# Optimization experiments

Hardware: AMD Instinct MI355X
Metric: run time of the kernel (lower is better)

Reference implementation:

```python
import jax, jax.numpy as jnp
import numpy as np

N, E, T = 50000, 200000, 100000
D, H, C = 512, 512, 7
BN_EPS = 1e-5


def _bn(h, g, b):
    # BatchNorm1d with batch statistics (training-mode stats, biased var as torch)
    m = jnp.mean(h, axis=0)
    v = jnp.var(h, axis=0)
    return (h - m) * jax.lax.rsqrt(v + BN_EPS) * g + b


def _forward(x, graph, edge_index, train_edge_id,
             W_sub, bn1_g, bn1_b, fcx_W, fcx_b, eps1,
             g_W1, g_b1, g_W2, g_b2, gbn_g, gbn_b,
             lin1_W, lin1_b, lin2_W, lin2_b, fc2_W, fc2_b):
    src, dst = edge_index[0], edge_index[1]
    n = x.shape[0]

    # SubgraphGNNKernel approximation: one GINConv (eps=0), mlp_layers=1 linear
    # (bias=False per bias=False), residual add (res=True)
    agg_s = graph + jax.ops.segment_sum(graph[src], dst, num_segments=n)
    sub_x = agg_s @ W_sub + graph  # [N, D]
    sub_x = jax.nn.relu(_bn(sub_x, bn1_g, bn1_b))  # dropout: eval no-op

    # fc_x
    h = x @ fcx_W + fcx_b  # [N, D]

    # GINConv: mlp((1+eps)*h + sum_{j->i} h_j)
    agg = (1.0 + eps1) * h + jax.ops.segment_sum(h[src], dst, num_segments=n)
    h = jax.nn.relu(agg @ g_W1 + g_b1)
    h = jax.nn.relu(h @ g_W2 + g_b2)
    h = _bn(h, gbn_g, gbn_b)  # [N, H]

    # lin1 -> relu -> (dropout eval no-op) -> lin2, add subgraph branch
    h = jax.nn.relu(h @ lin1_W + lin1_b)
    h = h @ lin2_W + lin2_b
    h = h + sub_x  # [N, H]

    # link prediction: gather endpoints of training edges, elementwise mul
    nid = edge_index[:, train_edge_id]  # [2, T]
    pair = h[nid[0]] * h[nid[1]]  # [T, H]
    return pair @ fc2_W + fc2_b  # [T, C]


def setup_inputs() -> dict:
    key = jax.random.key(0)
    ks = jax.random.split(key, 20)
    w = lambda k, shape: (jax.random.normal(k, shape, jnp.float32)
                          * (1.0 / np.sqrt(shape[0])))
    return {
        "x": jax.random.normal(ks[0], (N, D), jnp.float32),
        "graph": jax.random.normal(ks[1], (N, D), jnp.float32),
        "edge_index": jax.random.randint(ks[2], (2, E), 0, N),
        "train_edge_id": jax.random.randint(ks[3], (T,), 0, E),
        "W_sub": w(ks[4], (D, D)),
        "bn1_g": jnp.ones((D,), jnp.float32),
        "bn1_b": jnp.zeros((D,), jnp.float32),
        "fcx_W": w(ks[5], (D, D)),
        "fcx_b": jnp.zeros((D,), jnp.float32),
        "eps1": jnp.zeros((), jnp.float32),
        "g_W1": w(ks[6], (D, H)),
        "g_b1": jnp.zeros((H,), jnp.float32),
        "g_W2": w(ks[7], (H, H)),
        "g_b2": jnp.zeros((H,), jnp.float32),
        "gbn_g": jnp.ones((H,), jnp.float32),
        "gbn_b": jnp.zeros((H,), jnp.float32),
        "lin1_W": w(ks[8], (H, H)),
        "lin1_b": jnp.zeros((H,), jnp.float32),
        "lin2_W": w(ks[9], (H, H)),
        "lin2_b": jnp.zeros((H,), jnp.float32),
        "fc2_W": w(ks[10], (H, C)),
        "fc2_b": jnp.zeros((C,), jnp.float32),
    }


def reference(x, graph, edge_index, train_edge_id,
              W_sub, bn1_g, bn1_b, fcx_W, fcx_b, eps1,
              g_W1, g_b1, g_W2, g_b2, gbn_g, gbn_b,
              lin1_W, lin1_b, lin2_W, lin2_b, fc2_W, fc2_b):
    return _forward(x, graph, edge_index, train_edge_id,
                    W_sub, bn1_g, bn1_b, fcx_W, fcx_b, eps1,
                    g_W1, g_b1, g_W2, g_b2, gbn_g, gbn_b,
                    lin1_W, lin1_b, lin2_W, lin2_b, fc2_W, fc2_b)
```

## Files before the change

kernel.cpp:

```cpp
#include <hip/hip_runtime.h>

#define N_NODES 50000
#define N_EDGES 200000
#define N_TRAIN 100000
#define DIM     512
#define NCLS    7
#define NSB     ((N_NODES + 255) / 256)

typedef unsigned short ushort;
typedef _Float16 f16x8 __attribute__((ext_vector_type(8)));
typedef float    f32x4 __attribute__((ext_vector_type(4)));

__device__ __forceinline__ ushort f2h(float f) {
    _Float16 h = (_Float16)f;
    union { _Float16 h; ushort u; } v; v.h = h; return v.u;
}
__device__ __forceinline__ float h2f(ushort u) {
    union { ushort u; _Float16 h; } v; v.u = u; return (float)v.h;
}

__device__ __forceinline__ void gload_lds16(const void* g, void* l) {
    __builtin_amdgcn_global_load_lds((const __attribute__((address_space(1))) unsigned int*)g,
                                     (__attribute__((address_space(3))) unsigned int*)l,
                                     16, 0, 0);
}

#define VMWAIT(N) asm volatile("s_waitcnt vmcnt(" #N ")" ::: "memory")
#define LGKM0()   asm volatile("s_waitcnt lgkmcnt(0)" ::: "memory")
#define BAR() do { asm volatile("" ::: "memory"); __builtin_amdgcn_s_barrier(); \
                   asm volatile("" ::: "memory"); } while (0)


__global__ void zero_kernel(float* p, int n) {
    int i = blockIdx.x * blockDim.x + threadIdx.x;
    if (i < n) p[i] = 0.0f;
}


__global__ void hist_kernel(const int* __restrict__ ei, int* __restrict__ cnt) {
    int e = blockIdx.x * blockDim.x + threadIdx.x;
    if (e < N_EDGES) atomicAdd(&cnt[ei[N_EDGES + e]], 1);
}

__global__ __launch_bounds__(256) void scan1_kernel(const int* __restrict__ cnt,
                                                    int* __restrict__ off,
                                                    int* __restrict__ bsum) {
    __shared__ int s[256];
    int t = threadIdx.x, b = blockIdx.x;
    int i = b * 256 + t;
    s[t] = (i < N_NODES) ? cnt[i] : 0;
    __syncthreads();
    for (int d = 1; d < 256; d <<= 1) {
        int add = (t >= d) ? s[t - d] : 0;
        __syncthreads();
        s[t] += add;
        __syncthreads();
    }
    if (i < N_NODES) off[i + 1] = s[t];
    if (t == 255) bsum[b] = s[255];
}

__global__ __launch_bounds__(256) void scan2_kernel(int* bsum) {
    __shared__ int s[256];
    int t = threadIdx.x;
    s[t] = (t < NSB) ? bsum[t] : 0;
    __syncthreads();
    for (int d = 1; d < 256; d <<= 1) {
        int add = (t >= d) ? s[t - d] : 0;
        __syncthreads();
        s[t] += add;
        __syncthreads();
    }
    if (t < NSB) bsum[t] = s[t];
}

__global__ __launch_bounds__(256) void scan3_kernel(int* off, const int* __restrict__ bsum) {
    int t = threadIdx.x, b = blockIdx.x;
    int i = b * 256 + t;
    if (i == 0) off[0] = 0;
    if (i < N_NODES) off[i + 1] += (b > 0 ? bsum[b - 1] : 0);
}

__global__ void fillprep_kernel(const int* __restrict__ off, int* __restrict__ wcur) {
    int i = blockIdx.x * blockDim.x + threadIdx.x;
    if (i < N_NODES) wcur[i] = off[i];
}

__global__ void fill_kernel(const int* __restrict__ ei, int* __restrict__ wcur,
                            int* __restrict__ srclist) {
    int e = blockIdx.x * blockDim.x + threadIdx.x;
    if (e < N_EDGES) {
        int d = ei[N_EDGES + e];
        int pos = atomicAdd(&wcur[d], 1);
        srclist[pos] = ei[e];
    }
}


__global__ __launch_bounds__(128) void gather_h_kernel(const float* __restrict__ feat,
                                                       const float* __restrict__ base,
                                                       const float* eps_or_null,
                                                       const int* __restrict__ off,
                                                       const int* __restrict__ srclist,
                                                       ushort* __restrict__ oh) {
    int n = blockIdx.x;
    int t = threadIdx.x;
    float s = 1.0f;
    if (eps_or_null) s = 1.0f + *eps_or_null;
    int e0 = off[n], e1 = off[n + 1];
    float4 acc = ((const float4*)(base + (size_t)n * DIM))[t];
    acc.x *= s; acc.y *= s; acc.z *= s; acc.w *= s;
    for (int e = e0; e < e1; ++e) {
        int srcn = srclist[e];
        float4 v = ((const float4*)(feat + (size_t)srcn * DIM))[t];
        acc.x += v.x; acc.y += v.y; acc.z += v.z; acc.w += v.w;
    }
    size_t o = (size_t)n * DIM + t * 4;
    ushort4 r;
    r.x = f2h(acc.x); r.y = f2h(acc.y); r.z = f2h(acc.z); r.w = f2h(acc.w);
    *(ushort4*)(oh + o) = r;
}


__global__ __launch_bounds__(128) void gather_h16_kernel(const ushort* __restrict__ feat,
                                                         const ushort* __restrict__ base,
                                                         const float* eps_or_null,
                                                         const int* __restrict__ off,
                                                         const int* __restrict__ srclist,
                                                         ushort* __restrict__ oh) {
    int n = blockIdx.x;
    int t = threadIdx.x;
    float s = 1.0f;
    if (eps_or_null) s = 1.0f + *eps_or_null;
    int e0 = off[n], e1 = off[n + 1];
    ushort4 b4 = ((const ushort4*)(base + (size_t)n * DIM))[t];
    float4 acc;
    acc.x = h2f(b4.x) * s; acc.y = h2f(b4.y) * s;
    acc.z = h2f(b4.z) * s; acc.w = h2f(b4.w) * s;
    for (int e = e0; e < e1; ++e) {
        int srcn = srclist[e];
        ushort4 v = ((const ushort4*)(feat + (size_t)srcn * DIM))[t];
        acc.x += h2f(v.x); acc.y += h2f(v.y); acc.z += h2f(v.z); acc.w += h2f(v.w);
    }
    size_t o = (size_t)n * DIM + t * 4;
    ushort4 r;
    r.x = f2h(acc.x); r.y = f2h(acc.y); r.z = f2h(acc.z); r.w = f2h(acc.w);
    *(ushort4*)(oh + o) = r;
}

__global__ void convert_h_kernel(const float* __restrict__ X,
                                 ushort* __restrict__ oh, size_t n4) {
    size_t i = (size_t)blockIdx.x * blockDim.x + threadIdx.x;
    size_t stride = (size_t)gridDim.x * blockDim.x;
    const float4* X4 = (const float4*)X;
    for (; i < n4; i += stride) {
        float4 v = X4[i];
        ushort4 r;
        r.x = f2h(v.x); r.y = f2h(v.y); r.z = f2h(v.z); r.w = f2h(v.w);
        *(ushort4*)(oh + i * 4) = r;
    }
}

__global__ void wconvert6_kernel(const float* __restrict__ W0, const float* __restrict__ W1,
                                 const float* __restrict__ W2, const float* __restrict__ W3,
                                 const float* __restrict__ W4, const float* __restrict__ W5,
                                 ushort* __restrict__ wt) {
    int p = blockIdx.y;
    const float* W = (p == 0) ? W0 : (p == 1) ? W1 : (p == 2) ? W2
                   : (p == 3) ? W3 : (p == 4) ? W4 : W5;
    ushort* Th = wt + (size_t)p * 262144;
    int idx = blockIdx.x * 256 + threadIdx.x;
    int n = idx >> 9, k = idx & 511;
    Th[idx] = f2h(W[k * DIM + n]);
}

__global__ void wfold_kernel(const float* __restrict__ W1, const float* __restrict__ st2,
                             ushort* __restrict__ lw1s) {
    int idx = blockIdx.x * 256 + threadIdx.x;
    int n = idx >> 9, k = idx & 511;
    lw1s[idx] = f2h(W1[k * DIM + n] * st2[1024 + k]);
}

__global__ void bfold_kernel(const float* __restrict__ W1, const float* __restrict__ b1,
                             const float* __restrict__ st2, float* __restrict__ b1f) {
    int c = threadIdx.x;
    float s = 0.f;
#pragma unroll 8
    for (int k = 0; k < DIM; k++) s += st2[1536 + k] * W1[k * DIM + c];
    b1f[c] = b1[c] + s;
}


__global__ __launch_bounds__(512, 6) void gemm_f16_kernel(
    const ushort* __restrict__ Ahp0, const ushort* __restrict__ Wf0,
    const float* __restrict__ bias0, const float* __restrict__ amf0,
    const ushort* __restrict__ amh0, const float* __restrict__ bnst0,
    float* __restrict__ Cf0, ushort* __restrict__ Oh0, float* __restrict__ stats0,
    int relu0, int mode0,
    const ushort* __restrict__ Ahp1, const ushort* __restrict__ Wf1,
    const float* __restrict__ bias1, const float* __restrict__ amf1,
    const ushort* __restrict__ amh1, const float* __restrict__ bnst1,
    float* __restrict__ Cf1, ushort* __restrict__ Oh1, float* __restrict__ stats1,
    int relu1, int mode1,
    int M)
{
    __shared__ __align__(16) char smem[3 * 16384];

    const ushort* Ahp; const ushort* Wf; const float* bias; const float* addmat_f;
    const ushort* addmat_h; const float* bnst; float* Cf; ushort* Oh; float* stats;
    int relu, mode;
    if (blockIdx.y == 0) {
        Ahp = Ahp0; Wf = Wf0; bias = bias0; addmat_f = amf0; addmat_h = amh0;
        bnst = bnst0; Cf = Cf0; Oh = Oh0; stats = stats0; relu = relu0; mode = mode0;
    } else {
        Ahp = Ahp1; Wf = Wf1; bias = bias1; addmat_f = amf1; addmat_h = amh1;
        bnst = bnst1; Cf = Cf1; Oh = Oh1; stats = stats1; relu = relu1; mode = mode1;
    }

    int tid = threadIdx.x;
    int w = tid >> 6;
    int l = tid & 63;
    int wm = w >> 2;
    int wn = w & 3;

    int nwg = gridDim.x;
    int q = nwg >> 3, r = nwg & 7;
    int xcd = blockIdx.x & 7, idx = blockIdx.x >> 3;
    int wgid = (xcd < r ? xcd * (q + 1) : r * (q + 1) + (xcd - r) * q) + idx;
    int bm = (wgid >> 2) * 128;
    int bn = (wgid & 3) * 128;

    f32x4 acc[4][2];
#pragma unroll
    for (int i = 0; i < 4; i++)
#pragma unroll
        for (int j = 0; j < 2; j++) acc[i][j] = (f32x4){0.f, 0.f, 0.f, 0.f};

    int ro = l & 15;
    int co = l >> 4;

    size_t soff[2]; int lofs[2];
#pragma unroll
    for (int t2 = 0; t2 < 2; t2++) {
        int c = 2 * w + t2;
        int row0, base_; bool cl;
        if (c < 8) { row0 = c * 16;       base_ = bm; cl = true;  lofs[t2] = c * 1024; }
        else       { row0 = (c - 8) * 16; base_ = bn; cl = false; lofs[t2] = 8192 + (c - 8) * 1024; }
        int lrit = row0 + (l >> 2);
        int rr = base_ + lrit;
        if (cl) rr = min(rr, M - 1);
        int kc = (l & 3) ^ ((lrit >> 1) & 3);
        soff[t2] = (size_t)rr * DIM + kc * 8;
    }
    const ushort* sp0 = (2 * w < 8) ? Ahp : Wf;
    const ushort* sp1 = (2 * w + 1 < 8) ? Ahp : Wf;

    int aoff[4], woff[2];
#pragma unroll
    for (int i = 0; i < 4; i++) {
        int arow = wm * 64 + i * 16 + ro;
        aoff[i] = arow * 64 + ((co ^ ((arow >> 1) & 3)) << 4);
    }
#pragma unroll
    for (int j = 0; j < 2; j++) {
        int wrow = wn * 32 + j * 16 + ro;
        woff[j] = 8192 + wrow * 64 + ((co ^ ((wrow >> 1) & 3)) << 4);
    }

#define STAGE(BB, K0) do {                                                        \
    char* sb_ = smem + (BB) * 16384;                                              \
    gload_lds16(sp0 + soff[0] + (K0), sb_ + lofs[0]);                             \
    gload_lds16(sp1 + soff[1] + (K0), sb_ + lofs[1]);                             \
} while (0)

#define COMPUTE(BB) do {                                                          \
    const char* bb_ = (const char*)smem + (BB) * 16384;                           \
    f16x8 fa[4], fw2[2];                                                          \
    _Pragma("unroll")                                                             \
    for (int i = 0; i < 4; i++) fa[i] = *(const f16x8*)(bb_ + aoff[i]);           \
    _Pragma("unroll")                                                             \
    for (int j = 0; j < 2; j++) fw2[j] = *(const f16x8*)(bb_ + woff[j]);          \
    __builtin_amdgcn_s_setprio(1);                                                \
    _Pragma("unroll")                                                             \
    for (int i = 0; i < 4; i++)                                                   \
        _Pragma("unroll")                                                         \
        for (int j = 0; j < 2; j++)                                               \
            acc[i][j] = __builtin_amdgcn_mfma_f32_16x16x32_f16(fa[i], fw2[j], acc[i][j], 0, 0, 0); \
    __builtin_amdgcn_s_setprio(0);                                                \
} while (0)

    STAGE(0, 0);
    STAGE(1, 32);
    STAGE(2, 64);

    int bufi = 0;
    for (int ks = 0; ks < 16; ks++) {
        if (ks < 14)      { VMWAIT(4); }
        else if (ks == 14){ VMWAIT(2); }
        else              { VMWAIT(0); }
        BAR();
        COMPUTE(bufi);
        LGKM0();
        BAR();
        if (ks <= 12) STAGE(bufi, (ks + 3) * 32);
        bufi = (bufi == 2) ? 0 : bufi + 1;
    }

#undef STAGE
#undef COMPUTE

    int colbase = bn + wn * 32 + ro;
    int rowbase = bm + wm * 64 + co * 4;
    float sacc[2] = {0.f, 0.f};
    float qacc[2] = {0.f, 0.f};
#pragma unroll
    for (int j = 0; j < 2; j++) {
        int col = colbase + j * 16;
        float bi = bias ? bias[col] : 0.f;
        float sc = 0.f, sh = 0.f;
        if (bnst) { sc = bnst[1024 + col]; sh = bnst[1536 + col]; }
#pragma unroll
        for (int i = 0; i < 4; i++) {
#pragma unroll
            for (int rg = 0; rg < 4; rg++) {
                int row = rowbase + i * 16 + rg;
                if (row < M) {
                    float v = acc[i][j][rg] + bi;
                    if (addmat_f || addmat_h) {
                        float am = addmat_f ? addmat_f[(size_t)row * DIM + col]
                                            : h2f(addmat_h[(size_t)row * DIM + col]);
                        if (bnst) am = fmaxf(am * sc + sh, 0.f);
                        v += am;
                    }
                    if (relu) v = fmaxf(v, 0.f);
                    if (mode == 0) Cf[(size_t)row * DIM + col] = v;
                    else           Oh[(size_t)row * DIM + col] = f2h(v);
                    if (stats) { sacc[j] += v; qacc[j] += v * v; }
                }
            }
        }
    }
    if (stats) {
#pragma unroll
        for (int j = 0; j < 2; j++) {
            float ss = sacc[j], qq = qacc[j];
            ss += __shfl_xor(ss, 16); qq += __shfl_xor(qq, 16);
            ss += __shfl_xor(ss, 32); qq += __shfl_xor(qq, 32);
            if (co == 0) {
                int col = colbase + j * 16;
                atomicAdd(&stats[col], ss);
                atomicAdd(&stats[DIM + col], qq);
            }
        }
    }
}


__global__ void bn_finalize_kernel(float* st, const float* __restrict__ g,
                                   const float* __restrict__ b, int M) {
    int c = threadIdx.x;
    float mean = st[c] / (float)M;
    float var = st[DIM + c] / (float)M - mean * mean;
    float sc = g[c] * rsqrtf(var + 1e-5f);
    st[1024 + c] = sc;
    st[1536 + c] = b[c] - mean * sc;
}


__global__ __launch_bounds__(256) void pair_kernel(const ushort* __restrict__ H,
                                                   const int* __restrict__ ei,
                                                   const int* __restrict__ teid,
                                                   const float* __restrict__ W,
                                                   const float* __restrict__ bias,
                                                   float* __restrict__ out) {
    int lane = threadIdx.x & 63;
    int wid = blockIdx.x * 4 + (threadIdx.x >> 6);
    int nw = gridDim.x * 4;
    int d0 = lane * 8;

    float wreg[8][NCLS];
#pragma unroll
    for (int qd = 0; qd < 8; qd++)
#pragma unroll
        for (int c = 0; c < NCLS; c++)
            wreg[qd][c] = W[(d0 + qd) * NCLS + c];
    float bi[NCLS];
#pragma unroll
    for (int c = 0; c < NCLS; c++) bi[c] = bias[c];

    for (int t = wid; t < N_TRAIN; t += nw) {
        int id = teid[t];
        int n0 = ei[id];
        int n1 = ei[N_EDGES + id];
        f16x8 av = *(const f16x8*)(H + (size_t)n0 * DIM + d0);
        f16x8 bv = *(const f16x8*)(H + (size_t)n1 * DIM + d0);
        float acc[NCLS];
#pragma unroll
        for (int c = 0; c < NCLS; c++) acc[c] = 0.f;
#pragma unroll
        for (int qd = 0; qd < 8; qd++) {
            float p = (float)av[qd] * (float)bv[qd];
#pragma unroll
            for (int c = 0; c < NCLS; c++) acc[c] += p * wreg[qd][c];
        }
#pragma unroll
        for (int off = 32; off; off >>= 1)
#pragma unroll
            for (int c = 0; c < NCLS; c++) acc[c] += __shfl_down(acc[c], off);
        if (lane == 0) {
#pragma unroll
            for (int c = 0; c < NCLS; c++) out[(size_t)t * NCLS + c] = acc[c] + bi[c];
        }
    }
}


extern "C" void kernel_launch(void* const* d_in, const int* in_sizes, int n_in,
                              void* d_out, int out_size, void* d_ws, size_t ws_size,
                              hipStream_t stream) {
    const float* x      = (const float*)d_in[0];
    const float* graph  = (const float*)d_in[1];
    const int*   ei     = (const int*)d_in[2];
    const int*   teid   = (const int*)d_in[3];
    const float* W_sub  = (const float*)d_in[4];
    const float* bn1_g  = (const float*)d_in[5];
    const float* bn1_b  = (const float*)d_in[6];
    const float* fcx_W  = (const float*)d_in[7];
    const float* fcx_b  = (const float*)d_in[8];
    const float* eps1   = (const float*)d_in[9];
    const float* g_W1   = (const float*)d_in[10];
    const float* g_b1   = (const float*)d_in[11];
    const float* g_W2   = (const float*)d_in[12];
    const float* g_b2   = (const float*)d_in[13];
    const float* gbn_g  = (const float*)d_in[14];
    const float* gbn_b  = (const float*)d_in[15];
    const float* lin1_W = (const float*)d_in[16];
    const float* lin1_b = (const float*)d_in[17];
    const float* lin2_W = (const float*)d_in[18];
    const float* lin2_b = (const float*)d_in[19];
    const float* fc2_W  = (const float*)d_in[20];
    const float* fc2_b  = (const float*)d_in[21];
    float* out = (float*)d_out;

    char* ws = (char*)d_ws;
    size_t NB = (size_t)N_NODES * DIM * sizeof(float);
    float* slotA = (float*)(ws);
    float* slotB = (float*)(ws + NB);
    float* slotC = (float*)(ws + 2 * NB);
    float* st1   = (float*)(ws + 3 * NB);
    float* st2   = st1 + 2048;
    int* off     = (int*)(st2 + 2048);
    int* wcur    = off + (N_NODES + 1);
    int* srclist = wcur + N_NODES;
    int* bsum    = srclist + N_EDGES;
    ushort* wt   = (ushort*)(bsum + 256);
    ushort* Wsub_f = wt;
    ushort* fcx_f  = wt + 1 * 262144;
    ushort* gw1_f  = wt + 2 * 262144;
    ushort* gw2_f  = wt + 3 * 262144;
    ushort* lw2_f  = wt + 5 * 262144;
    ushort* lw1s   = wt + 6 * 262144;
    float*  b1f    = (float*)(lw1s + 262144);

    size_t HN = (size_t)N_NODES * DIM;
    ushort* A_h  = (ushort*)slotA;       ushort* A2_h = A_h + HN;
    ushort* B_h  = (ushort*)slotB;       ushort* B2_h = B_h + HN;
    ushort* C2_h = (ushort*)slotC;       ushort* H_h  = C2_h + HN;

    size_t n4 = HN / 4;
    int mt = (N_NODES + 127) / 128;
    dim3 ggrid(mt * 4);
    dim3 gdual(mt * 4, 2);

#define GEMM1ARG(A, W, B, AF, AH, BN, CF, OH, ST, RL, MD) \
    A, W, B, AF, AH, BN, CF, OH, ST, RL, MD, \
    (const ushort*)nullptr, (const ushort*)nullptr, (const float*)nullptr, \
    (const float*)nullptr, (const ushort*)nullptr, (const float*)nullptr, \
    (float*)nullptr, (ushort*)nullptr, (float*)nullptr, 0, 0, N_NODES

    zero_kernel<<<16, 256, 0, stream>>>(st1, 4096);
    zero_kernel<<<NSB, 256, 0, stream>>>((float*)wcur, N_NODES);

    hist_kernel<<<(N_EDGES + 255) / 256, 256, 0, stream>>>(ei, wcur);
    scan1_kernel<<<NSB, 256, 0, stream>>>(wcur, off, bsum);
    scan2_kernel<<<1, 256, 0, stream>>>(bsum);
    scan3_kernel<<<NSB, 256, 0, stream>>>(off, bsum);
    fillprep_kernel<<<NSB, 256, 0, stream>>>(off, wcur);
    fill_kernel<<<(N_EDGES + 255) / 256, 256, 0, stream>>>(ei, wcur, srclist);

    wconvert6_kernel<<<dim3(1024, 6), 256, 0, stream>>>(W_sub, fcx_W, g_W1, g_W2, lin1_W, lin2_W, wt);

    convert_h_kernel<<<2048, 256, 0, stream>>>(x, A2_h, n4);
    gather_h_kernel<<<N_NODES, 128, 0, stream>>>(graph, graph, nullptr, off, srclist, A_h);

    gemm_f16_kernel<<<gdual, 512, 0, stream>>>(
        A_h, Wsub_f, (const float*)nullptr, graph, (const ushort*)nullptr,
        (const float*)nullptr, (float*)nullptr, B_h, st1, 0, 1,
        A2_h, fcx_f, fcx_b, (const float*)nullptr, (const ushort*)nullptr,
        (const float*)nullptr, (float*)nullptr, C2_h, (float*)nullptr, 0, 1,
        N_NODES);
    bn_finalize_kernel<<<1, 512, 0, stream>>>(st1, bn1_g, bn1_b, N_NODES);

    gather_h16_kernel<<<N_NODES, 128, 0, stream>>>(C2_h, C2_h, eps1, off, srclist, A_h);

    gemm_f16_kernel<<<ggrid, 512, 0, stream>>>(GEMM1ARG(
        A_h, gw1_f, g_b1, (const float*)nullptr, (const ushort*)nullptr,
        (const float*)nullptr, (float*)nullptr, B2_h, (float*)nullptr, 1, 1));
    gemm_f16_kernel<<<ggrid, 512, 0, stream>>>(GEMM1ARG(
        B2_h, gw2_f, g_b2, (const float*)nullptr, (const ushort*)nullptr,
        (const float*)nullptr, (float*)nullptr, A2_h, st2, 1, 1));
    bn_finalize_kernel<<<1, 512, 0, stream>>>(st2, gbn_g, gbn_b, N_NODES);

    wfold_kernel<<<1024, 256, 0, stream>>>(lin1_W, st2, lw1s);
    bfold_kernel<<<1, 512, 0, stream>>>(lin1_W, lin1_b, st2, b1f);

    gemm_f16_kernel<<<ggrid, 512, 0, stream>>>(GEMM1ARG(
        A2_h, lw1s, b1f, (const float*)nullptr, (const ushort*)nullptr,
        (const float*)nullptr, (float*)nullptr, A_h, (float*)nullptr, 1, 1));
    gemm_f16_kernel<<<ggrid, 512, 0, stream>>>(GEMM1ARG(
        A_h, lw2_f, lin2_b, (const float*)nullptr, B_h,
        st1, (float*)nullptr, H_h, (float*)nullptr, 0, 1));

    pair_kernel<<<2048, 256, 0, stream>>>(H_h, ei, teid, fc2_W, fc2_b, out);

#undef GEMM1ARG
}
```

Before: 690.5 us.

## Split subgraph GEMM into three chunks co-scheduled with main-branch GEMMs

The W_sub GEMM of the subgraph branch is split row-wise into three chunks. Each chunk rides as the second grid slice (blockIdx.y==1) of the dual launches for g_W1, g_W2 and lin1, and the fcx GEMM becomes its own launch. The goal is to fill idle compute and tail waves in the sequential main-branch GEMMs and to remove one standalone GEMM launch. In exchange it adds a per-GEMM M bound with early exit, rearranges buffer aliasing, and moves the bn1 finalize later, which makes buffer reuse more fragile.

```diff
diff --git a/kernel.cpp b/kernel.cpp
--- a/kernel.cpp
+++ b/kernel.cpp
@@ -6,6 +6,10 @@
 #define DIM     512
 #define NCLS    7
 #define NSB     ((N_NODES + 255) / 256)
+
+#define M1A 16768
+#define M1B 16640
+#define M1C (N_NODES - M1A - M1B)
 
 typedef unsigned short ushort;
 typedef _Float16 f16x8 __attribute__((ext_vector_type(8)));
@@ -196,25 +200,26 @@
     const float* __restrict__ bias0, const float* __restrict__ amf0,
     const ushort* __restrict__ amh0, const float* __restrict__ bnst0,
     float* __restrict__ Cf0, ushort* __restrict__ Oh0, float* __restrict__ stats0,
-    int relu0, int mode0,
+    int relu0, int mode0, int M0,
     const ushort* __restrict__ Ahp1, const ushort* __restrict__ Wf1,
     const float* __restrict__ bias1, const float* __restrict__ amf1,
     const ushort* __restrict__ amh1, const float* __restrict__ bnst1,
     float* __restrict__ Cf1, ushort* __restrict__ Oh1, float* __restrict__ stats1,
-    int relu1, int mode1,
-    int M)
+    int relu1, int mode1, int M1)
 {
     __shared__ __align__(16) char smem[3 * 16384];
 
     const ushort* Ahp; const ushort* Wf; const float* bias; const float* addmat_f;
     const ushort* addmat_h; const float* bnst; float* Cf; ushort* Oh; float* stats;
-    int relu, mode;
+    int relu, mode, M;
     if (blockIdx.y == 0) {
         Ahp = Ahp0; Wf = Wf0; bias = bias0; addmat_f = amf0; addmat_h = amh0;
-        bnst = bnst0; Cf = Cf0; Oh = Oh0; stats = stats0; relu = relu0; mode = mode0;
+        bnst = bnst0; Cf = Cf0; Oh = Oh0; stats = stats0;
+        relu = relu0; mode = mode0; M = M0;
     } else {
         Ahp = Ahp1; Wf = Wf1; bias = bias1; addmat_f = amf1; addmat_h = amh1;
-        bnst = bnst1; Cf = Cf1; Oh = Oh1; stats = stats1; relu = relu1; mode = mode1;
+        bnst = bnst1; Cf = Cf1; Oh = Oh1; stats = stats1;
+        relu = relu1; mode = mode1; M = M1;
     }
 
     int tid = threadIdx.x;
@@ -229,6 +234,8 @@
     int wgid = (xcd < r ? xcd * (q + 1) : r * (q + 1) + (xcd - r) * q) + idx;
     int bm = (wgid >> 2) * 128;
     int bn = (wgid & 3) * 128;
+
+    if (bm >= M) return;
 
     f32x4 acc[4][2];
 #pragma unroll
@@ -463,20 +470,24 @@
     float*  b1f    = (float*)(lw1s + 262144);
 
     size_t HN = (size_t)N_NODES * DIM;
-    ushort* A_h  = (ushort*)slotA;       ushort* A2_h = A_h + HN;
+    ushort* A_h  = (ushort*)slotA;       ushort* X_h  = A_h + HN;   ushort* A2_h = X_h;
     ushort* B_h  = (ushort*)slotB;       ushort* B2_h = B_h + HN;
-    ushort* C2_h = (ushort*)slotC;       ushort* H_h  = C2_h + HN;
+    ushort* C2_h = (ushort*)slotC;       ushort* AG_h = C2_h + HN;  ushort* H_h  = AG_h;
 
     size_t n4 = HN / 4;
     int mt = (N_NODES + 127) / 128;
     dim3 ggrid(mt * 4);
     dim3 gdual(mt * 4, 2);
 
-#define GEMM1ARG(A, W, B, AF, AH, BN, CF, OH, ST, RL, MD) \
-    A, W, B, AF, AH, BN, CF, OH, ST, RL, MD, \
+    const ushort* G1A[3] = { A_h, A_h + (size_t)M1A * DIM, A_h + (size_t)(M1A + M1B) * DIM };
+    const float*  G1G[3] = { graph, graph + (size_t)M1A * DIM, graph + (size_t)(M1A + M1B) * DIM };
+    ushort*       G1O[3] = { B_h, B_h + (size_t)M1A * DIM, B_h + (size_t)(M1A + M1B) * DIM };
+    const int     G1M[3] = { M1A, M1B, M1C };
+
+#define NULLSET \
     (const ushort*)nullptr, (const ushort*)nullptr, (const float*)nullptr, \
     (const float*)nullptr, (const ushort*)nullptr, (const float*)nullptr, \
-    (float*)nullptr, (ushort*)nullptr, (float*)nullptr, 0, 0, N_NODES
+    (float*)nullptr, (ushort*)nullptr, (float*)nullptr, 0, 0, 0
 
     zero_kernel<<<16, 256, 0, stream>>>(st1, 4096);
     zero_kernel<<<NSB, 256, 0, stream>>>((float*)wcur, N_NODES);
@@ -489,39 +500,46 @@
     fill_kernel<<<(N_EDGES + 255) / 256, 256, 0, stream>>>(ei, wcur, srclist);
 
     wconvert6_kernel<<<dim3(1024, 6), 256, 0, stream>>>(W_sub, fcx_W, g_W1, g_W2, lin1_W, lin2_W, wt);
-
-    convert_h_kernel<<<2048, 256, 0, stream>>>(x, A2_h, n4);
+    convert_h_kernel<<<2048, 256, 0, stream>>>(x, X_h, n4);
     gather_h_kernel<<<N_NODES, 128, 0, stream>>>(graph, graph, nullptr, off, srclist, A_h);
 
+    gemm_f16_kernel<<<ggrid, 512, 0, stream>>>(
+        X_h, fcx_f, fcx_b, (const float*)nullptr, (const ushort*)nullptr,
+        (const float*)nullptr, (float*)nullptr, C2_h, (float*)nullptr, 0, 1, N_NODES,
+        NULLSET);
+
+    gather_h16_kernel<<<N_NODES, 128, 0, stream>>>(C2_h, C2_h, eps1, off, srclist, AG_h);
+
     gemm_f16_kernel<<<gdual, 512, 0, stream>>>(
-        A_h, Wsub_f, (const float*)nullptr, graph, (const ushort*)nullptr,
-        (const float*)nullptr, (float*)nullptr, B_h, st1, 0, 1,
-        A2_h, fcx_f, fcx_b, (const float*)nullptr, (const ushort*)nullptr,
-        (const float*)nullptr, (float*)nullptr, C2_h, (float*)nullptr, 0, 1,
-        N_NODES);
-    bn_finalize_kernel<<<1, 512, 0, stream>>>(st1, bn1_g, bn1_b, N_NODES);
-
-    gather_h16_kernel<<<N_NODES, 128, 0, stream>>>(C2_h, C2_h, eps1, off, srclist, A_h);
-
-    gemm_f16_kernel<<<ggrid, 512, 0, stream>>>(GEMM1ARG(
-        A_h, gw1_f, g_b1, (const float*)nullptr, (const ushort*)nullptr,
-        (const float*)nullptr, (float*)nullptr, B2_h, (float*)nullptr, 1, 1));
-    gemm_f16_kernel<<<ggrid, 512, 0, stream>>>(GEMM1ARG(
+        AG_h, gw1_f, g_b1, (const float*)nullptr, (const ushort*)nullptr,
+        (const float*)nullptr, (float*)nullptr, B2_h, (float*)nullptr, 1, 1, N_NODES,
+        G1A[0], Wsub_f, (const float*)nullptr, G1G[0], (const ushort*)nullptr,
+        (const float*)nullptr, (float*)nullptr, G1O[0], st1, 0, 1, G1M[0]);
+
+    gemm_f16_kernel<<<gdual, 512, 0, stream>>>(
         B2_h, gw2_f, g_b2, (const float*)nullptr, (const ushort*)nullptr,
-        (const float*)nullptr, (float*)nullptr, A2_h, st2, 1, 1));
+        (const float*)nullptr, (float*)nullptr, A2_h, st2, 1, 1, N_NODES,
+        G1A[1], Wsub_f, (const float*)nullptr, G1G[1], (const ushort*)nullptr,
+        (const float*)nullptr, (float*)nullptr, G1O[1], st1, 0, 1, G1M[1]);
+
     bn_finalize_kernel<<<1, 512, 0, stream>>>(st2, gbn_g, gbn_b, N_NODES);
-
     wfold_kernel<<<1024, 256, 0, stream>>>(lin1_W, st2, lw1s);
     bfold_kernel<<<1, 512, 0, stream>>>(lin1_W, lin1_b, st2, b1f);
 
-    gemm_f16_kernel<<<ggrid, 512, 0, stream>>>(GEMM1ARG(
+    gemm_f16_kernel<<<gdual, 512, 0, stream>>>(
         A2_h, lw1s, b1f, (const float*)nullptr, (const ushort*)nullptr,
-        (const float*)nullptr, (float*)nullptr, A_h, (float*)nullptr, 1, 1));
-    gemm_f16_kernel<<<ggrid, 512, 0, stream>>>(GEMM1ARG(
-        A_h, lw2_f, lin2_b, (const float*)nullptr, B_h,
-        st1, (float*)nullptr, H_h, (float*)nullptr, 0, 1));
+        (const float*)nullptr, (float*)nullptr, C2_h, (float*)nullptr, 1, 1, N_NODES,
+        G1A[2], Wsub_f, (const float*)nullptr, G1G[2], (const ushort*)nullptr,
+        (const float*)nullptr, (float*)nullptr, G1O[2], st1, 0, 1, G1M[2]);
+
+    bn_finalize_kernel<<<1, 512, 0, stream>>>(st1, bn1_g, bn1_b, N_NODES);
+
+    gemm_f16_kernel<<<ggrid, 512, 0, stream>>>(
+        C2_h, lw2_f, lin2_b, (const float*)nullptr, B_h,
+        st1, (float*)nullptr, H_h, (float*)nullptr, 0, 1, N_NODES,
+        NULLSET);
 
     pair_kernel<<<2048, 256, 0, stream>>>(H_h, ei, teid, fc2_W, fc2_b, out);
 
-#undef GEMM1ARG
-}
+#undef NULLSET
+}
```

After: 905.9 us. 1.31x slower.
